# Kernel tuning notes

Measured on AMD Instinct MI355X. Metric: run time of the kernel, lower is better.

## Reference

```python
import jax, jax.numpy as jnp
import numpy as np

NEG = -1e30


def setup_inputs() -> dict:
    key = jax.random.key(0)
    ks = jax.random.split(key, 8)
    B, d, Lc, Lq = 32, 128, 2048, 512
    C = jax.random.normal(ks[0], (B, d, Lc), dtype=jnp.float32)
    Q = jax.random.normal(ks[1], (B, d, Lq), dtype=jnp.float32)
    Cmask = jax.random.randint(ks[2], (B, Lc), 0, 2, dtype=jnp.int32)
    Qmask = jax.random.randint(ks[3], (B, Lq), 0, 2, dtype=jnp.int32)
    # xavier_uniform over (d, 1): bound = sqrt(6 / (d + 1))
    bnd = float(np.sqrt(6.0 / (d + 1)))
    w_c = jax.random.uniform(ks[4], (d, 1), minval=-bnd, maxval=bnd, dtype=jnp.float32)
    w_q = jax.random.uniform(ks[5], (d, 1), minval=-bnd, maxval=bnd, dtype=jnp.float32)
    bnd_m = float(np.sqrt(6.0 / (1 + d)))
    w_mul = jax.random.uniform(ks[6], (1, 1, d), minval=-bnd_m, maxval=bnd_m, dtype=jnp.float32)
    bias = jnp.zeros((1,), dtype=jnp.float32)
    return {"C": C, "Q": Q, "Cmask": Cmask, "Qmask": Qmask,
            "w_c": w_c, "w_q": w_q, "w_mul": w_mul, "bias": bias}


def reference(C, Q, Cmask, Qmask, w_c, w_q, w_mul, bias):
    # C: [B, d, Lc], Q: [B, d, Lq] -> transpose to token-major
    Ct = jnp.swapaxes(C, 1, 2)  # [B, Lc, d]
    Qt = jnp.swapaxes(Q, 1, 2)  # [B, Lq, d]
    cm = Cmask.astype(jnp.float32)[:, :, None]   # [B, Lc, 1]
    qm = Qmask.astype(jnp.float32)[:, None, :]   # [B, 1, Lq]
    # optimized trilinear similarity S: [B, Lc, Lq] (dropout p=0 / eval mode)
    s0 = Ct @ w_c                                  # [B, Lc, 1]
    s1 = jnp.swapaxes(Qt @ w_q, 1, 2)              # [B, 1, Lq]
    s2 = jnp.einsum('bcd,bqd->bcq', Ct * w_mul, Qt)  # [B, Lc, Lq]
    S = s0 + s1 + s2 + bias
    S1 = jax.nn.softmax(S + NEG * (1.0 - qm), axis=2)  # mask over query axis
    S2 = jax.nn.softmax(S + NEG * (1.0 - cm), axis=1)  # mask over context axis
    A = jnp.einsum('bcq,bqd->bcd', S1, Qt)             # [B, Lc, d]
    Bm = jnp.einsum('bck,bkd->bcd', jnp.einsum('bcq,bkq->bck', S1, S2), Ct)
    out = jnp.concatenate([Ct, A, Ct * A, Ct * Bm], axis=2)  # [B, Lc, 4d]
    return jnp.swapaxes(out, 1, 2)  # [B, 4d, Lc]
```

## Files before the change

kernel.cpp:

```cpp
#include <hip/hip_runtime.h>

#define B_ 32
#define D_ 128
#define LC 2048
#define LQ 512
#define CCH 16

#define NEGINF (-3.0e38f)

typedef __attribute__((ext_vector_type(8))) short bf16x8;
typedef __attribute__((ext_vector_type(4))) float f32x4;
typedef __attribute__((ext_vector_type(8))) unsigned short us8;
typedef __attribute__((ext_vector_type(8))) _Float16 f16x8;

__device__ __forceinline__ unsigned short bf16rne(float x) {
    unsigned int u = __float_as_uint(x);
    u = (u + 0x7FFFu + ((u >> 16) & 1u)) >> 16;
    return (unsigned short)u;
}

__device__ __forceinline__ void gll16(const void* g, void* l) {
    __builtin_amdgcn_global_load_lds((const __attribute__((address_space(1))) void*)g,
                                     (__attribute__((address_space(3))) void*)l, 16, 0, 0);
}

__global__ void k_dotw(const float* __restrict__ X, const float* __restrict__ w,
                       float* __restrict__ outv, int L) {
    int idx = blockIdx.x * 256 + threadIdx.x;
    int b = idx / L, x = idx - b * L;
    const float* Xp = X + (size_t)b * D_ * L + x;
    float acc = 0.f;
#pragma unroll 8
    for (int dd = 0; dd < D_; ++dd) acc += Xp[(size_t)dd * L] * w[dd];
    outv[idx] = acc;
}

__global__ void k_prep_C(const float* __restrict__ C, const float* __restrict__ wmul,
                         short* __restrict__ Ctw, short* __restrict__ Cb16) {
    int b = blockIdx.y, c0 = blockIdx.x * 64;
    __shared__ float Tf[128][65];
    __shared__ float wm[128];
    int t = threadIdx.x;
    if (t < 128) wm[t] = wmul[t];
    const float* Cb = C + (size_t)b * D_ * LC;
#pragma unroll
    for (int i = 0; i < 8; ++i) {
        int idx = t + i * 256;
        int d = idx >> 4, c4 = idx & 15;
        float4 v = *(const float4*)(Cb + (size_t)d * LC + c0 + c4 * 4);
        Tf[d][c4 * 4 + 0] = v.x; Tf[d][c4 * 4 + 1] = v.y;
        Tf[d][c4 * 4 + 2] = v.z; Tf[d][c4 * 4 + 3] = v.w;
        ushort4 cv;
        cv.x = bf16rne(v.x); cv.y = bf16rne(v.y); cv.z = bf16rne(v.z); cv.w = bf16rne(v.w);
        *(ushort4*)(Cb16 + ((size_t)b * D_ + d) * LC + c0 + c4 * 4) = cv;
    }
    __syncthreads();
    int c_l = t & 63, g = t >> 6;
    unsigned short u[32];
#pragma unroll
    for (int j = 0; j < 32; ++j) {
        int d = g * 32 + j;
        u[j] = bf16rne(Tf[d][c_l] * wm[d]);
    }
    short* dst = Ctw + ((size_t)b * LC + c0 + c_l) * D_ + g * 32;
#pragma unroll
    for (int k = 0; k < 4; ++k) *(us8*)(dst + k * 8) = *(const us8*)&u[k * 8];
}

__global__ void k_prep_Q(const float* __restrict__ Q, short* __restrict__ Qt16,
                         short* __restrict__ Wf) {
    int b = blockIdx.y, q0 = blockIdx.x * 64;
    __shared__ float Tf[128][65];
    int t = threadIdx.x;
    const float* Qb = Q + (size_t)b * D_ * LQ;
#pragma unroll
    for (int i = 0; i < 8; ++i) {
        int idx = t + i * 256;
        int d = idx >> 4, q4 = idx & 15;
        float4 v = *(const float4*)(Qb + (size_t)d * LQ + q0 + q4 * 4);
        Tf[d][q4 * 4 + 0] = v.x; Tf[d][q4 * 4 + 1] = v.y;
        Tf[d][q4 * 4 + 2] = v.z; Tf[d][q4 * 4 + 3] = v.w;
        ushort4 cv;
        cv.x = bf16rne(v.x); cv.y = bf16rne(v.y); cv.z = bf16rne(v.z); cv.w = bf16rne(v.w);
        *(ushort4*)(Wf + ((size_t)b * 256 + d) * LQ + q0 + q4 * 4) = cv;
    }
    __syncthreads();
    int q_l = t & 63, g = t >> 6;
    unsigned short u[32];
#pragma unroll
    for (int j = 0; j < 32; ++j) u[j] = bf16rne(Tf[g * 32 + j][q_l]);
    short* dst = Qt16 + ((size_t)b * LQ + q0 + q_l) * D_ + g * 32;
#pragma unroll
    for (int k = 0; k < 4; ++k) *(us8*)(dst + k * 8) = *(const us8*)&u[k * 8];
}

__global__ __launch_bounds__(256) void k_S_mfma(const short* __restrict__ Ctw,
                                                const short* __restrict__ Qt16,
                                                const float* __restrict__ s0,
                                                const float* __restrict__ s1,
                                                const float* __restrict__ bias,
                                                _Float16* __restrict__ S16) {
    int b = blockIdx.y;
    int cT = blockIdx.x >> 2, qT = blockIdx.x & 3;
    int c0 = cT * 128, q0 = qT * 128;
    int t = threadIdx.x, w = t >> 6, l = t & 63;
    int wm_ = w >> 1, wn = w & 1;
    __shared__ short As[128 * 64];
    __shared__ short Bs[128 * 64];
    f32x4 acc[4][4] = {};
    const short* Arow = Ctw + ((size_t)b * LC + c0) * D_;
    const short* Brow = Qt16 + ((size_t)b * LQ + q0) * D_;
    int lr = l >> 3, sl = l & 7;
    for (int kt = 0; kt < 2; ++kt) {
        __syncthreads();
#pragma unroll
        for (int i = 0; i < 4; ++i) {
            int r = w * 32 + i * 8 + lr;
            int g = sl ^ (r & 7);
            gll16(Arow + (size_t)r * D_ + kt * 64 + g * 8, &As[(w * 32 + i * 8) * 64]);
            gll16(Brow + (size_t)r * D_ + kt * 64 + g * 8, &Bs[(w * 32 + i * 8) * 64]);
        }
        __syncthreads();
#pragma unroll
        for (int ks = 0; ks < 2; ++ks) {
            int kg = ks * 4 + (l >> 4);
            bf16x8 af[4], bfr[4];
#pragma unroll
            for (int ms = 0; ms < 4; ++ms) {
                int m = wm_ * 64 + ms * 16 + (l & 15);
                af[ms] = *(const bf16x8*)&As[m * 64 + (kg ^ (m & 7)) * 8];
            }
#pragma unroll
            for (int ns = 0; ns < 4; ++ns) {
                int n = wn * 64 + ns * 16 + (l & 15);
                bfr[ns] = *(const bf16x8*)&Bs[n * 64 + (kg ^ (n & 7)) * 8];
            }
#pragma unroll
            for (int ms = 0; ms < 4; ++ms)
#pragma unroll
                for (int ns = 0; ns < 4; ++ns)
                    acc[ms][ns] = __builtin_amdgcn_mfma_f32_16x16x32_bf16(af[ms], bfr[ns], acc[ms][ns], 0, 0, 0);
        }
    }
    float bv = bias[0];
#pragma unroll
    for (int ms = 0; ms < 4; ++ms) {
        int cb = c0 + wm_ * 64 + ms * 16 + (l >> 4) * 4;
#pragma unroll
        for (int ns = 0; ns < 4; ++ns) {
            int q = q0 + wn * 64 + ns * 16 + (l & 15);
            float s1v = s1[b * LQ + q] + bv;
#pragma unroll
            for (int r = 0; r < 4; ++r) {
                int c = cb + r;
                S16[((size_t)b * LC + c) * LQ + q] = (_Float16)(acc[ms][ns][r] + s0[b * LC + c] + s1v);
            }
        }
    }
}

__global__ void k_rowstats(const _Float16* __restrict__ S16, const int* __restrict__ Qmask,
                           float* __restrict__ rowmax, float* __restrict__ rowsum) {
    int row = blockIdx.x * 4 + (threadIdx.x >> 6);
    int lane = threadIdx.x & 63;
    int b = row / LC;
    f16x8 v = *(const f16x8*)(S16 + (size_t)row * LQ + lane * 8);
    const int* qm = Qmask + b * LQ + lane * 8;
    int4 m0 = *(const int4*)qm;
    int4 m1 = *(const int4*)(qm + 4);
    int mk[8] = {m0.x, m0.y, m0.z, m0.w, m1.x, m1.y, m1.z, m1.w};
    float vf[8];
#pragma unroll
    for (int k = 0; k < 8; ++k) vf[k] = (float)v[k];
    float mx = NEGINF;
#pragma unroll
    for (int k = 0; k < 8; ++k) if (mk[k]) mx = fmaxf(mx, vf[k]);
#pragma unroll
    for (int off = 32; off > 0; off >>= 1) mx = fmaxf(mx, __shfl_xor(mx, off, 64));
    float s = 0.f;
#pragma unroll
    for (int k = 0; k < 8; ++k) if (mk[k]) s += __expf(vf[k] - mx);
#pragma unroll
    for (int off = 32; off > 0; off >>= 1) s += __shfl_xor(s, off, 64);
    if (lane == 0) { rowmax[row] = mx; rowsum[row] = s; }
}

__global__ __launch_bounds__(256) void k_colstats_part(const _Float16* __restrict__ S16,
                                                       const int* __restrict__ Cmask,
                                                       float* __restrict__ pm,
                                                       float* __restrict__ pl) {
    int b = blockIdx.y;
    int q0 = blockIdx.x * 64;
    int ch = blockIdx.z;
    int t = threadIdx.x, ql = t & 63, cg = t >> 6;
    const int cbase = ch * (LC / CCH);
    const _Float16* Sb = S16 + (size_t)b * LC * LQ + (size_t)cbase * LQ + q0 + ql;
    const int* cm = Cmask + b * LC + cbase;
    float v[32];
#pragma unroll
    for (int i = 0; i < 32; ++i) {
        int c = cg + 4 * i;
        float x = (float)Sb[(size_t)c * LQ];
        v[i] = cm[c] ? x : NEGINF;
    }
    float m8[8];
#pragma unroll
    for (int j = 0; j < 8; ++j) m8[j] = v[j];
#pragma unroll
    for (int i = 8; i < 32; ++i) m8[i & 7] = fmaxf(m8[i & 7], v[i]);
    float m = fmaxf(fmaxf(fmaxf(m8[0], m8[1]), fmaxf(m8[2], m8[3])),
                    fmaxf(fmaxf(m8[4], m8[5]), fmaxf(m8[6], m8[7])));
    float s8[8];
#pragma unroll
    for (int j = 0; j < 8; ++j) s8[j] = 0.f;
#pragma unroll
    for (int i = 0; i < 32; ++i) s8[i & 7] += __expf(v[i] - m);
    float l = ((s8[0] + s8[1]) + (s8[2] + s8[3])) + ((s8[4] + s8[5]) + (s8[6] + s8[7]));
    if (m == NEGINF) l = 0.f;
    __shared__ float Ms[4][64], Ls[4][64];
    Ms[cg][ql] = m; Ls[cg][ql] = l;
    __syncthreads();
    if (t < 64) {
        float mm = Ms[0][ql], ll = Ls[0][ql];
#pragma unroll
        for (int g = 1; g < 4; ++g) {
            float m2 = Ms[g][ql], l2 = Ls[g][ql];
            float mn = fmaxf(mm, m2);
            ll = ll * __expf(mm - mn) + l2 * __expf(m2 - mn);
            mm = mn;
        }
        size_t o = ((size_t)ch * B_ + b) * LQ + q0 + ql;
        pm[o] = mm; pl[o] = ll;
    }
}

__global__ void k_colstats_comb(const float* __restrict__ pm, const float* __restrict__ pl,
                                float* __restrict__ colmax, float* __restrict__ colsum) {
    int idx = blockIdx.x * 256 + threadIdx.x;
    float m = NEGINF, l = 0.f;
#pragma unroll
    for (int ch = 0; ch < CCH; ++ch) {
        float m2 = pm[(size_t)ch * B_ * LQ + idx];
        float l2 = pl[(size_t)ch * B_ * LQ + idx];
        float mn = fmaxf(m, m2);
        l = l * __expf(m - mn) + l2 * __expf(m2 - mn);
        m = mn;
    }
    colmax[idx] = m; colsum[idx] = l;
}

__global__ __launch_bounds__(256) void k_V2_mfma(const short* __restrict__ Cb16,
                                                 const _Float16* __restrict__ S16,
                                                 const int* __restrict__ Cmask,
                                                 const float* __restrict__ colmax,
                                                 const float* __restrict__ colsum,
                                                 short* __restrict__ Wf) {
    int b = blockIdx.y;
    int q0 = blockIdx.x * 64;
    int t = threadIdx.x, w = t >> 6, l = t & 63;
    __shared__ short As[128 * 64];
    __shared__ short Bs[64 * 72];
    f32x4 acc[2][4] = {};
    const short* Arow = Cb16 + (size_t)b * D_ * LC;
    int lr = l >> 3, sl = l & 7;
    float cmx[16];
#pragma unroll
    for (int j2 = 0; j2 < 4; ++j2)
        *(float4*)&cmx[j2 * 4] = *(const float4*)(colmax + b * LQ + q0 + w * 16 + j2 * 4);
    const _Float16* Sq = S16 + (size_t)b * LC * LQ + q0 + w * 16;
    const int* cmb = Cmask + b * LC;

    for (int kt = 0; kt < 32; ++kt) {
        int ck = kt * 64;
        __syncthreads();
#pragma unroll
        for (int i = 0; i < 4; ++i) {
            int r = w * 32 + i * 8 + lr;
            int g = sl ^ (r & 7);
            gll16(Arow + (size_t)r * LC + ck + g * 8, &As[(w * 32 + i * 8) * 64]);
        }
        {
            float cmf = (float)cmb[ck + l];
            const _Float16* sp = Sq + (size_t)(ck + l) * LQ;
            f16x8 v0 = *(const f16x8*)sp;
            f16x8 v1 = *(const f16x8*)(sp + 8);
#pragma unroll
            for (int j = 0; j < 8; ++j)
                Bs[(w * 16 + j) * 72 + l] = (short)bf16rne(cmf * __expf((float)v0[j] - cmx[j]));
#pragma unroll
            for (int j = 0; j < 8; ++j)
                Bs[(w * 16 + 8 + j) * 72 + l] = (short)bf16rne(cmf * __expf((float)v1[j] - cmx[8 + j]));
        }
        __syncthreads();
#pragma unroll
        for (int ks = 0; ks < 2; ++ks) {
            int kg = ks * 4 + (l >> 4);
            bf16x8 af[2], bfr[4];
#pragma unroll
            for (int ms = 0; ms < 2; ++ms) {
                int m = w * 32 + ms * 16 + (l & 15);
                af[ms] = *(const bf16x8*)&As[m * 64 + (kg ^ (m & 7)) * 8];
            }
#pragma unroll
            for (int ns = 0; ns < 4; ++ns) {
                int n = ns * 16 + (l & 15);
                bfr[ns] = *(const bf16x8*)&Bs[n * 72 + kg * 8];
            }
#pragma unroll
            for (int ms = 0; ms < 2; ++ms)
#pragma unroll
                for (int ns = 0; ns < 4; ++ns)
                    acc[ms][ns] = __builtin_amdgcn_mfma_f32_16x16x32_bf16(af[ms], bfr[ns], acc[ms][ns], 0, 0, 0);
        }
    }
#pragma unroll
    for (int ms = 0; ms < 2; ++ms)
#pragma unroll
        for (int ns = 0; ns < 4; ++ns) {
            int q = q0 + ns * 16 + (l & 15);
            float csi = 1.0f / colsum[b * LQ + q];
#pragma unroll
            for (int r = 0; r < 4; ++r) {
                int dd = w * 32 + ms * 16 + (l >> 4) * 4 + r;
                Wf[((size_t)b * 256 + 128 + dd) * LQ + q] = (short)bf16rne(acc[ms][ns][r] * csi);
            }
        }
}

__global__ __launch_bounds__(256) void k_out_mfma(const _Float16* __restrict__ S16,
                                                  const short* __restrict__ Wf,
                                                  const float* __restrict__ C,
                                                  const int* __restrict__ Qmask,
                                                  const float* __restrict__ rowmax,
                                                  const float* __restrict__ rowsum,
                                                  float* __restrict__ out) {
    int b = blockIdx.y;
    int cT = blockIdx.x >> 1, nT = blockIdx.x & 1;
    int c0 = cT * 128;
    int t = threadIdx.x, w = t >> 6, l = t & 63;
    int wm_ = w >> 1, wc = w & 1;
    __shared__ short As[128 * 64];
    __shared__ short Bs[128 * 72];
    f32x4 acc[4][4] = {};
    int br = t >> 1, bh = t & 1;
    float rm = rowmax[b * LC + c0 + br];
    float ri = 1.0f / rowsum[b * LC + c0 + br];
    const _Float16* Srow = S16 + ((size_t)b * LC + c0 + br) * LQ;
    const int* qmb = Qmask + b * LQ;
    const short* Arow = Wf + ((size_t)b * 256 + nT * 128) * LQ;
    int lr = l >> 3, sl = l & 7;
    for (int kt = 0; kt < 8; ++kt) {
        int qk = kt * 64;
        __syncthreads();
#pragma unroll
        for (int i = 0; i < 4; ++i) {
            int r = w * 32 + i * 8 + lr;
            int g = sl ^ (r & 7);
            gll16(Arow + (size_t)r * LQ + qk + g * 8, &As[(w * 32 + i * 8) * 64]);
        }
#pragma unroll
        for (int j2 = 0; j2 < 4; ++j2) {
            int qo = qk + bh * 32 + j2 * 8;
            f16x8 v = *(const f16x8*)(Srow + qo);
            int4 qa = *(const int4*)(qmb + qo);
            int4 qb = *(const int4*)(qmb + qo + 4);
            unsigned short u[8];
            u[0] = qa.x ? bf16rne(__expf((float)v[0] - rm) * ri) : (unsigned short)0;
            u[1] = qa.y ? bf16rne(__expf((float)v[1] - rm) * ri) : (unsigned short)0;
            u[2] = qa.z ? bf16rne(__expf((float)v[2] - rm) * ri) : (unsigned short)0;
            u[3] = qa.w ? bf16rne(__expf((float)v[3] - rm) * ri) : (unsigned short)0;
            u[4] = qb.x ? bf16rne(__expf((float)v[4] - rm) * ri) : (unsigned short)0;
            u[5] = qb.y ? bf16rne(__expf((float)v[5] - rm) * ri) : (unsigned short)0;
            u[6] = qb.z ? bf16rne(__expf((float)v[6] - rm) * ri) : (unsigned short)0;
            u[7] = qb.w ? bf16rne(__expf((float)v[7] - rm) * ri) : (unsigned short)0;
            *(us8*)&Bs[br * 72 + bh * 32 + j2 * 8] = *(const us8*)&u[0];
        }
        __syncthreads();
#pragma unroll
        for (int ks = 0; ks < 2; ++ks) {
            int kg = ks * 4 + (l >> 4);
            bf16x8 af[4], bfr[4];
#pragma unroll
            for (int ms = 0; ms < 4; ++ms) {
                int m = wm_ * 64 + ms * 16 + (l & 15);
                af[ms] = *(const bf16x8*)&As[m * 64 + (kg ^ (m & 7)) * 8];
            }
#pragma unroll
            for (int ns = 0; ns < 4; ++ns) {
                int cc = wc * 64 + ns * 16 + (l & 15);
                bfr[ns] = *(const bf16x8*)&Bs[cc * 72 + kg * 8];
            }
#pragma unroll
            for (int ms = 0; ms < 4; ++ms)
#pragma unroll
                for (int ns = 0; ns < 4; ++ns)
                    acc[ms][ns] = __builtin_amdgcn_mfma_f32_16x16x32_bf16(af[ms], bfr[ns], acc[ms][ns], 0, 0, 0);
        }
    }
#pragma unroll
    for (int ms = 0; ms < 4; ++ms) {
        int nb = nT * 128 + wm_ * 64 + ms * 16 + (l >> 4) * 4;
#pragma unroll
        for (int ns = 0; ns < 4; ++ns) {
            int c = c0 + wc * 64 + ns * 16 + (l & 15);
#pragma unroll
            for (int r = 0; r < 4; ++r) {
                int n = nb + r;
                float a = acc[ms][ns][r];
                if (n < 128) {
                    float cv = C[((size_t)b * D_ + n) * LC + c];
                    out[((size_t)b * 512 + 128 + n) * LC + c] = a;
                    out[((size_t)b * 512 + 256 + n) * LC + c] = cv * a;
                } else {
                    int dd = n - 128;
                    float cv = C[((size_t)b * D_ + dd) * LC + c];
                    out[((size_t)b * 512 + 384 + dd) * LC + c] = cv * a;
                }
            }
        }
    }
}

__global__ void k_copy(const float* __restrict__ C, float* __restrict__ out) {
    int idx = blockIdx.x * 256 + threadIdx.x;
    const int perB = D_ * LC / 4;
    int b = idx / perB, r = idx - b * perB;
    const float4* src = (const float4*)(C + (size_t)b * D_ * LC);
    float4* dst = (float4*)(out + (size_t)b * 4 * D_ * LC);
    dst[r] = src[r];
}

extern "C" void kernel_launch(void* const* d_in, const int* in_sizes, int n_in,
                              void* d_out, int out_size, void* d_ws, size_t ws_size,
                              hipStream_t stream) {
    const float* C     = (const float*)d_in[0];
    const float* Q     = (const float*)d_in[1];
    const int*   Cmask = (const int*)d_in[2];
    const int*   Qmask = (const int*)d_in[3];
    const float* w_c   = (const float*)d_in[4];
    const float* w_q   = (const float*)d_in[5];
    const float* w_mul = (const float*)d_in[6];
    const float* bias  = (const float*)d_in[7];
    float* out = (float*)d_out;

    _Float16* S16 = (_Float16*)d_ws;
    short* Cb16 = (short*)(S16 + (size_t)B_ * LC * LQ);
    short* Ctw  = Cb16 + (size_t)B_ * D_ * LC;
    short* Qt16 = Ctw + (size_t)B_ * LC * D_;
    short* Wf   = Qt16 + (size_t)B_ * LQ * D_;
    float* s0     = (float*)(Wf + (size_t)B_ * 256 * LQ);
    float* s1     = s0 + B_ * LC;
    float* rowmax = s1 + B_ * LQ;
    float* rowsum = rowmax + B_ * LC;
    float* colmax = rowsum + B_ * LC;
    float* colsum = colmax + B_ * LQ;
    float* pm     = colsum + B_ * LQ;
    float* pl     = pm + (size_t)CCH * B_ * LQ;

    hipLaunchKernelGGL(k_dotw, dim3(B_ * LC / 256), dim3(256), 0, stream, C, w_c, s0, LC);
    hipLaunchKernelGGL(k_dotw, dim3(B_ * LQ / 256), dim3(256), 0, stream, Q, w_q, s1, LQ);
    hipLaunchKernelGGL(k_prep_C, dim3(LC / 64, B_), dim3(256), 0, stream, C, w_mul, Ctw, Cb16);
    hipLaunchKernelGGL(k_prep_Q, dim3(LQ / 64, B_), dim3(256), 0, stream, Q, Qt16, Wf);
    hipLaunchKernelGGL(k_S_mfma, dim3((LC / 128) * (LQ / 128), B_), dim3(256), 0, stream,
                       Ctw, Qt16, s0, s1, bias, S16);
    hipLaunchKernelGGL(k_rowstats, dim3(B_ * LC / 4), dim3(256), 0, stream, S16, Qmask, rowmax, rowsum);
    hipLaunchKernelGGL(k_colstats_part, dim3(LQ / 64, B_, CCH), dim3(256), 0, stream,
                       S16, Cmask, pm, pl);
    hipLaunchKernelGGL(k_colstats_comb, dim3(B_ * LQ / 256), dim3(256), 0, stream,
                       pm, pl, colmax, colsum);
    hipLaunchKernelGGL(k_V2_mfma, dim3(LQ / 64, B_), dim3(256), 0, stream,
                       Cb16, S16, Cmask, colmax, colsum, Wf);
    hipLaunchKernelGGL(k_out_mfma, dim3((LC / 128) * 2, B_), dim3(256), 0, stream,
                       S16, Wf, C, Qmask, rowmax, rowsum, out);
    hipLaunchKernelGGL(k_copy, dim3(B_ * D_ * LC / 4 / 256), dim3(256), 0, stream, C, out);
}
```

Measured before the change: 428.8 us.

## Materialize row softmax in place as bf16 and fuse C copy into output kernel

The row-stats kernel now writes the normalized, masked row softmax back into the S buffer as bf16, and it runs after the column-softmax consumer. The output GEMM can then stream P1 through async global-to-LDS loads with a swizzled layout, instead of recomputing exp per element inside the K loop. The separate copy kernel for the first D rows of the output is removed, and those writes are folded into the output epilogue. The trade-off is an extra read/write pass over S, and the C-copy stores in the epilogue are strided rather than vectorized.

Measured after the change: 412.1 us. 3.9% less time.

```diff
diff --git a/kernel.cpp b/kernel.cpp
--- a/kernel.cpp
+++ b/kernel.cpp
@@ -159,12 +159,12 @@
     }
 }
 
-__global__ void k_rowstats(const _Float16* __restrict__ S16, const int* __restrict__ Qmask,
-                           float* __restrict__ rowmax, float* __restrict__ rowsum) {
+__global__ void k_rowsoftmax(_Float16* __restrict__ S16, const int* __restrict__ Qmask) {
     int row = blockIdx.x * 4 + (threadIdx.x >> 6);
     int lane = threadIdx.x & 63;
     int b = row / LC;
-    f16x8 v = *(const f16x8*)(S16 + (size_t)row * LQ + lane * 8);
+    _Float16* Sp = S16 + (size_t)row * LQ + lane * 8;
+    f16x8 v = *(const f16x8*)Sp;
     const int* qm = Qmask + b * LQ + lane * 8;
     int4 m0 = *(const int4*)qm;
     int4 m1 = *(const int4*)(qm + 4);
@@ -177,12 +177,17 @@
     for (int k = 0; k < 8; ++k) if (mk[k]) mx = fmaxf(mx, vf[k]);
 #pragma unroll
     for (int off = 32; off > 0; off >>= 1) mx = fmaxf(mx, __shfl_xor(mx, off, 64));
+    float e[8];
     float s = 0.f;
 #pragma unroll
-    for (int k = 0; k < 8; ++k) if (mk[k]) s += __expf(vf[k] - mx);
+    for (int k = 0; k < 8; ++k) { e[k] = __expf(vf[k] - mx); if (mk[k]) s += e[k]; }
 #pragma unroll
     for (int off = 32; off > 0; off >>= 1) s += __shfl_xor(s, off, 64);
-    if (lane == 0) { rowmax[row] = mx; rowsum[row] = s; }
+    float ri = 1.0f / s;
+    unsigned short u[8];
+#pragma unroll
+    for (int k = 0; k < 8; ++k) u[k] = mk[k] ? bf16rne(e[k] * ri) : (unsigned short)0;
+    *(us8*)Sp = *(const us8*)&u[0];
 }
 
 __global__ __launch_bounds__(256) void k_colstats_part(const _Float16* __restrict__ S16,
@@ -327,12 +332,9 @@
         }
 }
 
-__global__ __launch_bounds__(256) void k_out_mfma(const _Float16* __restrict__ S16,
+__global__ __launch_bounds__(256) void k_out_mfma(const short* __restrict__ P1,
                                                   const short* __restrict__ Wf,
                                                   const float* __restrict__ C,
-                                                  const int* __restrict__ Qmask,
-                                                  const float* __restrict__ rowmax,
-                                                  const float* __restrict__ rowsum,
                                                   float* __restrict__ out) {
     int b = blockIdx.y;
     int cT = blockIdx.x >> 1, nT = blockIdx.x & 1;
@@ -340,40 +342,19 @@
     int t = threadIdx.x, w = t >> 6, l = t & 63;
     int wm_ = w >> 1, wc = w & 1;
     __shared__ short As[128 * 64];
-    __shared__ short Bs[128 * 72];
+    __shared__ short Bs[128 * 64];
     f32x4 acc[4][4] = {};
-    int br = t >> 1, bh = t & 1;
-    float rm = rowmax[b * LC + c0 + br];
-    float ri = 1.0f / rowsum[b * LC + c0 + br];
-    const _Float16* Srow = S16 + ((size_t)b * LC + c0 + br) * LQ;
-    const int* qmb = Qmask + b * LQ;
     const short* Arow = Wf + ((size_t)b * 256 + nT * 128) * LQ;
+    const short* Brow = P1 + ((size_t)b * LC + c0) * LQ;
     int lr = l >> 3, sl = l & 7;
     for (int kt = 0; kt < 8; ++kt) {
-        int qk = kt * 64;
         __syncthreads();
 #pragma unroll
         for (int i = 0; i < 4; ++i) {
             int r = w * 32 + i * 8 + lr;
             int g = sl ^ (r & 7);
-            gll16(Arow + (size_t)r * LQ + qk + g * 8, &As[(w * 32 + i * 8) * 64]);
-        }
-#pragma unroll
-        for (int j2 = 0; j2 < 4; ++j2) {
-            int qo = qk + bh * 32 + j2 * 8;
-            f16x8 v = *(const f16x8*)(Srow + qo);
-            int4 qa = *(const int4*)(qmb + qo);
-            int4 qb = *(const int4*)(qmb + qo + 4);
-            unsigned short u[8];
-            u[0] = qa.x ? bf16rne(__expf((float)v[0] - rm) * ri) : (unsigned short)0;
-            u[1] = qa.y ? bf16rne(__expf((float)v[1] - rm) * ri) : (unsigned short)0;
-            u[2] = qa.z ? bf16rne(__expf((float)v[2] - rm) * ri) : (unsigned short)0;
-            u[3] = qa.w ? bf16rne(__expf((float)v[3] - rm) * ri) : (unsigned short)0;
-            u[4] = qb.x ? bf16rne(__expf((float)v[4] - rm) * ri) : (unsigned short)0;
-            u[5] = qb.y ? bf16rne(__expf((float)v[5] - rm) * ri) : (unsigned short)0;
-            u[6] = qb.z ? bf16rne(__expf((float)v[6] - rm) * ri) : (unsigned short)0;
-            u[7] = qb.w ? bf16rne(__expf((float)v[7] - rm) * ri) : (unsigned short)0;
-            *(us8*)&Bs[br * 72 + bh * 32 + j2 * 8] = *(const us8*)&u[0];
+            gll16(Arow + (size_t)r * LQ + kt * 64 + g * 8, &As[(w * 32 + i * 8) * 64]);
+            gll16(Brow + (size_t)r * LQ + kt * 64 + g * 8, &Bs[(w * 32 + i * 8) * 64]);
         }
         __syncthreads();
 #pragma unroll
@@ -388,7 +369,7 @@
 #pragma unroll
             for (int ns = 0; ns < 4; ++ns) {
                 int cc = wc * 64 + ns * 16 + (l & 15);
-                bfr[ns] = *(const bf16x8*)&Bs[cc * 72 + kg * 8];
+                bfr[ns] = *(const bf16x8*)&Bs[cc * 64 + (kg ^ (cc & 7)) * 8];
             }
 #pragma unroll
             for (int ms = 0; ms < 4; ++ms)
@@ -409,6 +390,7 @@
                 float a = acc[ms][ns][r];
                 if (n < 128) {
                     float cv = C[((size_t)b * D_ + n) * LC + c];
+                    out[((size_t)b * 512 + n) * LC + c] = cv;
                     out[((size_t)b * 512 + 128 + n) * LC + c] = a;
                     out[((size_t)b * 512 + 256 + n) * LC + c] = cv * a;
                 } else {
@@ -419,15 +401,6 @@
             }
         }
     }
-}
-
-__global__ void k_copy(const float* __restrict__ C, float* __restrict__ out) {
-    int idx = blockIdx.x * 256 + threadIdx.x;
-    const int perB = D_ * LC / 4;
-    int b = idx / perB, r = idx - b * perB;
-    const float4* src = (const float4*)(C + (size_t)b * D_ * LC);
-    float4* dst = (float4*)(out + (size_t)b * 4 * D_ * LC);
-    dst[r] = src[r];
 }
 
 extern "C" void kernel_launch(void* const* d_in, const int* in_sizes, int n_in,
@@ -456,6 +429,7 @@
     float* colsum = colmax + B_ * LQ;
     float* pm     = colsum + B_ * LQ;
     float* pl     = pm + (size_t)CCH * B_ * LQ;
+    (void)rowmax; (void)rowsum;
 
     hipLaunchKernelGGL(k_dotw, dim3(B_ * LC / 256), dim3(256), 0, stream, C, w_c, s0, LC);
     hipLaunchKernelGGL(k_dotw, dim3(B_ * LQ / 256), dim3(256), 0, stream, Q, w_q, s1, LQ);
@@ -463,14 +437,13 @@
     hipLaunchKernelGGL(k_prep_Q, dim3(LQ / 64, B_), dim3(256), 0, stream, Q, Qt16, Wf);
     hipLaunchKernelGGL(k_S_mfma, dim3((LC / 128) * (LQ / 128), B_), dim3(256), 0, stream,
                        Ctw, Qt16, s0, s1, bias, S16);
-    hipLaunchKernelGGL(k_rowstats, dim3(B_ * LC / 4), dim3(256), 0, stream, S16, Qmask, rowmax, rowsum);
     hipLaunchKernelGGL(k_colstats_part, dim3(LQ / 64, B_, CCH), dim3(256), 0, stream,
                        S16, Cmask, pm, pl);
     hipLaunchKernelGGL(k_colstats_comb, dim3(B_ * LQ / 256), dim3(256), 0, stream,
                        pm, pl, colmax, colsum);
     hipLaunchKernelGGL(k_V2_mfma, dim3(LQ / 64, B_), dim3(256), 0, stream,
                        Cb16, S16, Cmask, colmax, colsum, Wf);
+    hipLaunchKernelGGL(k_rowsoftmax, dim3(B_ * LC / 4), dim3(256), 0, stream, S16, Qmask);
     hipLaunchKernelGGL(k_out_mfma, dim3((LC / 128) * 2, B_), dim3(256), 0, stream,
-                       S16, Wf, C, Qmask, rowmax, rowsum, out);
-    hipLaunchKernelGGL(k_copy, dim3(B_ * D_ * LC / 4 / 256), dim3(256), 0, stream, C, out);
-}
+                       (const short*)S16, Wf, C, out);
+}
```
